# Kernel tuning notes

Hardware: AMD Instinct MI355X
Metric: run time of the kernel (lower is better)

Reference implementation:

```python
import jax, jax.numpy as jnp
import numpy as np

B, N, C, L, H = 8, 128, 64, 3, 128  # batch, objects, channels, eq-layers, message hidden
NEG_SLOPE = 0.01  # torch leaky_relu default


def setup_inputs() -> dict:
    key = jax.random.key(0)
    ks = jax.random.split(key, 10)
    def p(k, shape, fan):
        return jax.random.normal(k, shape, dtype=jnp.float32) * np.float32(np.sqrt(2.0 / fan))
    return {
        "x": jax.random.normal(ks[0], (B, N, N, C), dtype=jnp.float32),
        "mask": jnp.ones((B, N, N, 1), dtype=jnp.float32),
        # MessageNet per eq-layer: Linear(C->H), Linear(H->H), Linear(H->C), stacked over L layers
        "msg_w1": p(ks[1], (L, H, C), C + H),
        "msg_b1": jnp.zeros((L, H), jnp.float32),
        "msg_w2": p(ks[2], (L, H, H), H + H),
        "msg_b2": jnp.zeros((L, H), jnp.float32),
        "msg_w3": p(ks[3], (L, C, H), H + C),
        "msg_b3": jnp.zeros((L, C), jnp.float32),
        # Eq2to2 params: coefs (in_dim, out_dim, 15), bias, diag_bias
        "coefs": p(ks[4], (L, C, C, 15), C + C + 15),
        "bias": jnp.zeros((L, C), jnp.float32),
        "diag_bias": jnp.zeros((L, C), jnp.float32),
    }


def leaky(x):
    return jax.nn.leaky_relu(x, NEG_SLOPE)


def eops_2_to_2(x):
    # x: (B, m, m, C) -> ops: (B, C, 15, m, m); aggregation='sum'
    t = jnp.transpose(x, (0, 3, 1, 2))            # (B, C, m, m)
    m = t.shape[-1]
    eye = jnp.eye(m, dtype=t.dtype)
    diag = jnp.diagonal(t, axis1=-2, axis2=-1)    # (B, C, m)
    sum_diag = diag.sum(-1, keepdims=True)        # (B, C, 1)
    sum_rows = t.sum(-1)                          # (B, C, m)  sum over j
    sum_cols = t.sum(-2)                          # (B, C, m)  sum over i
    sum_all = t.sum((-2, -1))[..., None]          # (B, C, 1)
    de = lambda v: v[..., :, None] * eye          # diag_embed with broadcast
    shp = t.shape
    bc = lambda a: jnp.broadcast_to(a, shp)
    ops = [
        de(diag),                                 # 1  diag -> diag
        de(sum_diag),                             # 2  trace -> diag
        de(sum_rows),                             # 3  row sums -> diag
        de(sum_cols),                             # 4  col sums -> diag
        de(sum_all),                              # 5  total sum -> diag
        bc(sum_cols[..., :, None]),               # 6  col sums broadcast over j
        bc(sum_rows[..., :, None]),               # 7  row sums broadcast over j
        bc(sum_cols[..., None, :]),               # 8  col sums broadcast over i
        bc(sum_rows[..., None, :]),               # 9  row sums broadcast over i
        t,                                        # 10 identity
        jnp.swapaxes(t, -2, -1),                  # 11 transpose
        bc(diag[..., :, None]),                   # 12 diag broadcast over j
        bc(diag[..., None, :]),                   # 13 diag broadcast over i
        bc(sum_diag[..., :, None]),               # 14 trace broadcast everywhere
        bc(sum_all[..., :, None]),                # 15 total sum broadcast everywhere
    ]
    return jnp.stack(ops, axis=2)                 # (B, C, 15, m, m)


def reference(x, mask, msg_w1, msg_b1, msg_w2, msg_b2, msg_w3, msg_b3, coefs, bias, diag_bias):
    m = x.shape[1]
    eye = jnp.eye(m, dtype=x.dtype)[None, :, :, None]  # (1, m, m, 1)
    for l in range(L):
        # MessageNet: pointwise MLP over channels, activation after each linear, then mask
        h = leaky(jnp.einsum('nijc,hc->nijh', x, msg_w1[l]) + msg_b1[l])
        h = leaky(jnp.einsum('nijc,hc->nijh', h, msg_w2[l]) + msg_b2[l])
        h = leaky(jnp.einsum('nijc,hc->nijh', h, msg_w3[l]) + msg_b3[l])
        h = h * mask
        # Eq2to2
        ops = eops_2_to_2(h)                              # (B, C, 15, m, m)
        out = jnp.einsum('dsb,ndbij->nijs', coefs[l], ops)
        out = out + bias[l][None, None, None, :] + eye * diag_bias[l][None, None, None, :]
        out = leaky(out)
        x = out * mask
    return x
```

## Files before the change

kernel.cpp:

```cpp
#include <hip/hip_runtime.h>
#include <hip/hip_bf16.h>

#define BB 8
#define NN 128
#define CC 64
#define LL 3
#define HH 128
#define NEG 0.01f
#define NPOS (BB*NN*NN)

typedef __attribute__((ext_vector_type(8))) short shortx8;
typedef __attribute__((ext_vector_type(4))) float f32x4;

#define OFF_HHI   0L
#define OFF_XN    8388608L
#define OFF_RS    12582912L
#define OFF_DG    12648448L
#define OFF_RCDH  12713984L
#define OFF_RCDL  12812288L
#define OFF_U     12911616L
#define OFF_V     12977152L
#define OFF_D     13042688L
#define OFF_SB    13108224L

__device__ __forceinline__ float leaky(float v) { return v >= 0.f ? v : NEG * v; }

__device__ __forceinline__ short f2bf(float f) {
    return (short)__bfloat16_as_ushort(__float2bfloat16(f));
}
__device__ __forceinline__ float bf2f(short s) {
    unsigned u = ((unsigned)(unsigned short)s) << 16;
    return __builtin_bit_cast(float, u);
}
__device__ __forceinline__ unsigned pkf(float a, float b) {
    return (unsigned)(unsigned short)f2bf(a) | ((unsigned)(unsigned short)f2bf(b) << 16);
}
__device__ __forceinline__ shortx8 cvt8(const float* p) {
    float4 f0 = *(const float4*)p, f1 = *(const float4*)(p + 4);
    shortx8 r;
    r[0]=f2bf(f0.x); r[1]=f2bf(f0.y); r[2]=f2bf(f0.z); r[3]=f2bf(f0.w);
    r[4]=f2bf(f1.x); r[5]=f2bf(f1.y); r[6]=f2bf(f1.z); r[7]=f2bf(f1.w);
    return r;
}

__global__ void prep_kernel(const float* __restrict__ w1, const float* __restrict__ w2,
                            const float* __restrict__ w3, const float* __restrict__ coefs,
                            float* __restrict__ ws) {
    long idx = (long)blockIdx.x * 256 + threadIdx.x;
    short* sb = (short*)(ws + OFF_SB);
    if (idx < 24576) {
        sb[idx] = f2bf(w1[idx]);
    } else if (idx < 73728) {
        sb[idx] = f2bf(w2[idx - 24576]);
    } else if (idx < 98304) {
        sb[idx] = f2bf(w3[idx - 73728]);
    } else if (idx < 110592) {
        long r = idx - 98304; int l = (int)(r / 4096); int q = (int)(r % 4096);
        int s = q >> 6, d = q & 63;
        float v = coefs[(((long)l*CC + d)*CC + s)*15 + 9];
        short hi = f2bf(v);
        sb[98304 + r]  = hi;
        sb[110592 + r] = f2bf(v - bf2f(hi));
    } else if (idx < 122880) {
        long r = idx - 110592; int l = (int)(r / 4096); int q = (int)(r % 4096);
        int s = q >> 6, d = q & 63;
        float v = coefs[(((long)l*CC + d)*CC + s)*15 + 10];
        short hi = f2bf(v);
        sb[122880 + r] = hi;
        sb[135168 + r] = f2bf(v - bf2f(hi));
    } else if (idx < 233472) {
        long r = idx - 122880;
        int l = (int)(r / 36864); int q = (int)(r % 36864);
        int o = q / 192, k = q % 192;
        int wo = o >> 6, s = o & 63, wk = k >> 6, d = k & 63;
        const int sel[3][3] = {{5,6,11},{7,8,12},{3,2,0}};
        float v = coefs[(((long)l*CC + d)*CC + s)*15 + sel[wo][wk]];
        short hi = f2bf(v);
        sb[147456 + r] = hi;
        sb[258048 + r] = f2bf(v - bf2f(hi));
    }
}

__global__ __launch_bounds__(256, 5) void mlp_kernel(
    const float* __restrict__ xf, const short* __restrict__ xb,
    const float* __restrict__ mask,
    const float* __restrict__ b1, const float* __restrict__ b2, const float* __restrict__ b3,
    const short* __restrict__ wb1, const short* __restrict__ wb2, const short* __restrict__ wb3,
    short* __restrict__ hout)
{
    __shared__ __align__(16) char lds[32768];
    const int t = threadIdx.x;
    const int lane = t & 63;
    const int w = t >> 6;
    const int arow = lane & 15;
    const int kgrp = lane >> 4;
    const long pos0 = (long)blockIdx.x * 64;
    const int XT = 16384;

    {
        const int row = t >> 2, q = t & 3;
        const long off = (pos0 + row)*CC + q*16;
        shortx8 v0, v1;
        if (xb) { v0 = *(const shortx8*)(xb + off); v1 = *(const shortx8*)(xb + off + 8); }
        else    { v0 = cvt8(xf + off);              v1 = cvt8(xf + off + 8); }
        const int swz = (row & 7) << 4;
        *(shortx8*)(&lds[XT + row*128 + ((q*32)      ^ swz)]) = v0;
        *(shortx8*)(&lds[XT + row*128 + ((q*32 + 16) ^ swz)]) = v1;
    }
    __syncthreads();

    {
        f32x4 acc[2][4];
        #pragma unroll
        for (int of = 0; of < 2; ++of)
            #pragma unroll
            for (int pf = 0; pf < 4; ++pf) acc[of][pf] = (f32x4){0.f,0.f,0.f,0.f};
        #pragma unroll
        for (int kk = 0; kk < 2; ++kk) {
            shortx8 bx[4];
            #pragma unroll
            for (int pf = 0; pf < 4; ++pf) {
                const int p = pf*16 + arow;
                bx[pf] = *(const shortx8*)(&lds[XT + p*128 + ((kk*64 + kgrp*16) ^ ((p & 7) << 4))]);
            }
            #pragma unroll
            for (int of = 0; of < 2; ++of) {
                const shortx8 a = *(const shortx8*)(wb1 + (long)(w*32 + of*16 + arow)*CC + kk*32 + kgrp*8);
                #pragma unroll
                for (int pf = 0; pf < 4; ++pf)
                    acc[of][pf] = __builtin_amdgcn_mfma_f32_16x16x32_bf16(a, bx[pf], acc[of][pf], 0, 0, 0);
            }
        }
        #pragma unroll
        for (int of = 0; of < 2; ++of) {
            const int o0 = w*32 + of*16 + kgrp*4;
            const float4 bv = *(const float4*)(b1 + o0);
            #pragma unroll
            for (int pf = 0; pf < 4; ++pf) {
                const int p = pf*16 + arow;
                unsigned u0 = pkf(leaky(acc[of][pf][0] + bv.x), leaky(acc[of][pf][1] + bv.y));
                unsigned u1 = pkf(leaky(acc[of][pf][2] + bv.z), leaky(acc[of][pf][3] + bv.w));
                *(uint2*)(&lds[p*256 + ((o0*2) ^ ((p & 15) << 4))]) = make_uint2(u0, u1);
            }
        }
    }
    __syncthreads();

    {
        f32x4 acc[2][4];
        #pragma unroll
        for (int of = 0; of < 2; ++of)
            #pragma unroll
            for (int pf = 0; pf < 4; ++pf) acc[of][pf] = (f32x4){0.f,0.f,0.f,0.f};
        #pragma unroll
        for (int kk = 0; kk < 4; ++kk) {
            shortx8 bx[4];
            #pragma unroll
            for (int pf = 0; pf < 4; ++pf) {
                const int p = pf*16 + arow;
                bx[pf] = *(const shortx8*)(&lds[p*256 + ((kk*64 + kgrp*16) ^ ((p & 15) << 4))]);
            }
            #pragma unroll
            for (int of = 0; of < 2; ++of) {
                const shortx8 a = *(const shortx8*)(wb2 + (long)(w*32 + of*16 + arow)*HH + kk*32 + kgrp*8);
                #pragma unroll
                for (int pf = 0; pf < 4; ++pf)
                    acc[of][pf] = __builtin_amdgcn_mfma_f32_16x16x32_bf16(a, bx[pf], acc[of][pf], 0, 0, 0);
            }
        }
        __syncthreads();
        #pragma unroll
        for (int of = 0; of < 2; ++of) {
            const int o0 = w*32 + of*16 + kgrp*4;
            const float4 bv = *(const float4*)(b2 + o0);
            #pragma unroll
            for (int pf = 0; pf < 4; ++pf) {
                const int p = pf*16 + arow;
                unsigned u0 = pkf(leaky(acc[of][pf][0] + bv.x), leaky(acc[of][pf][1] + bv.y));
                unsigned u1 = pkf(leaky(acc[of][pf][2] + bv.z), leaky(acc[of][pf][3] + bv.w));
                *(uint2*)(&lds[16384 + p*256 + ((o0*2) ^ ((p & 15) << 4))]) = make_uint2(u0, u1);
            }
        }
    }
    __syncthreads();

    {
        f32x4 acc[4];
        #pragma unroll
        for (int pf = 0; pf < 4; ++pf) acc[pf] = (f32x4){0.f,0.f,0.f,0.f};
        #pragma unroll
        for (int kk = 0; kk < 4; ++kk) {
            const shortx8 a = *(const shortx8*)(wb3 + (long)(w*16 + arow)*HH + kk*32 + kgrp*8);
            #pragma unroll
            for (int pf = 0; pf < 4; ++pf) {
                const int p = pf*16 + arow;
                const shortx8 bx = *(const shortx8*)(&lds[16384 + p*256 + ((kk*64 + kgrp*16) ^ ((p & 15) << 4))]);
                acc[pf] = __builtin_amdgcn_mfma_f32_16x16x32_bf16(a, bx, acc[pf], 0, 0, 0);
            }
        }
        const int o0 = w*16 + kgrp*4;
        const float4 bv = *(const float4*)(b3 + o0);
        #pragma unroll
        for (int pf = 0; pf < 4; ++pf) {
            const int p = pf*16 + arow;
            const long pos = pos0 + p;
            const float mv = mask[pos];
            float v0 = leaky(acc[pf][0] + bv.x) * mv;
            float v1 = leaky(acc[pf][1] + bv.y) * mv;
            float v2 = leaky(acc[pf][2] + bv.z) * mv;
            float v3 = leaky(acc[pf][3] + bv.w) * mv;
            *(uint2*)(hout + pos*CC + o0) = make_uint2(pkf(v0, v1), pkf(v2, v3));
        }
    }
}

__global__ __launch_bounds__(256) void reduce_kernel(const short* __restrict__ h,
                                                     float* __restrict__ rowsum,
                                                     float* __restrict__ diag,
                                                     short* __restrict__ rcdh,
                                                     short* __restrict__ rcdl) {
    const int br = blockIdx.x;
    const int n = br >> 7, r = br & 127;
    const int t = threadIdx.x;
    const int c8 = (t & 7) * 8;
    const int g = t >> 3;
    __shared__ float red[32][64];
    const long rowbase = ((long)(n*NN + r) * NN) * CC;

    {
        float s[8];
        #pragma unroll
        for (int e = 0; e < 8; ++e) s[e] = 0.f;
        for (int j = g; j < NN; j += 32) {
            const shortx8 vh = *(const shortx8*)(h + rowbase + (long)j*CC + c8);
            #pragma unroll
            for (int e = 0; e < 8; ++e) s[e] += bf2f(vh[e]);
        }
        #pragma unroll
        for (int e = 0; e < 8; ++e) red[g][c8 + e] = s[e];
    }
    __syncthreads();
    if (t < 64) {
        float rs = 0.f;
        #pragma unroll
        for (int k = 0; k < 32; ++k) rs += red[k][t];
        rowsum[(long)br*CC + t] = rs;
        short hh = f2bf(rs);
        rcdh[(long)br*192 + 64 + t] = hh;
        rcdl[(long)br*192 + 64 + t] = f2bf(rs - bf2f(hh));
    }
    __syncthreads();

    {
        const long colbase = ((long)n*NN*NN + r) * CC;
        float s[8];
        #pragma unroll
        for (int e = 0; e < 8; ++e) s[e] = 0.f;
        for (int i = g; i < NN; i += 32) {
            const shortx8 vh = *(const shortx8*)(h + colbase + (long)i*NN*CC + c8);
            #pragma unroll
            for (int e = 0; e < 8; ++e) s[e] += bf2f(vh[e]);
        }
        #pragma unroll
        for (int e = 0; e < 8; ++e) red[g][c8 + e] = s[e];
    }
    __syncthreads();
    if (t < 64) {
        float cs = 0.f;
        #pragma unroll
        for (int k = 0; k < 32; ++k) cs += red[k][t];
        short hh = f2bf(cs);
        rcdh[(long)br*192 + t] = hh;
        rcdl[(long)br*192 + t] = f2bf(cs - bf2f(hh));
        const float dg = bf2f(h[rowbase + (long)r*CC + t]);
        diag[(long)br*CC + t] = dg;
        short hd = f2bf(dg);
        rcdh[(long)br*192 + 128 + t] = hd;
        rcdl[(long)br*192 + 128 + t] = f2bf(dg - bf2f(hd));
    }
}

__global__ __launch_bounds__(256) void uvd_kernel(
    const short* __restrict__ rcdh, const short* __restrict__ rcdl,
    const short* __restrict__ kh, const short* __restrict__ kl,
    const float* __restrict__ rowsum, const float* __restrict__ diag,
    const float* __restrict__ coefs, int layer,
    float* __restrict__ U, float* __restrict__ V, float* __restrict__ D)
{
    __shared__ float ra[4][64], rb[4][64];
    __shared__ float ub[64], db[64];
    const int t = threadIdx.x, lane = t & 63, w = t >> 6;
    const int arow = lane & 15, kgrp = lane >> 4;
    const int r0 = blockIdx.x * 64;
    const int nb = r0 >> 7;

    {
        const int c = t & 63, g = t >> 6;
        float a = 0.f, b = 0.f;
        for (int i = g; i < NN; i += 4) {
            a += rowsum[((long)nb*NN + i)*CC + c];
            b += diag[((long)nb*NN + i)*CC + c];
        }
        ra[g][c] = a; rb[g][c] = b;
    }
    __syncthreads();
    if (t < 128) {
        const int which = t >> 6, s = t & 63;
        const float* cf = coefs + (long)layer*CC*CC*15;
        float acc = 0.f;
        for (int d = 0; d < CC; ++d) {
            const float tt = ra[0][d] + ra[1][d] + ra[2][d] + ra[3][d];
            const float tr = rb[0][d] + rb[1][d] + rb[2][d] + rb[3][d];
            const float* cds = cf + ((long)d*CC + s)*15;
            if (which == 0) acc += cds[13]*tr + cds[14]*tt;
            else            acc += cds[1]*tr + cds[4]*tt;
        }
        if (which == 0) ub[s] = acc; else db[s] = acc;
    }
    __syncthreads();

    f32x4 acc[3][4];
    #pragma unroll
    for (int o = 0; o < 3; ++o)
        #pragma unroll
        for (int pf = 0; pf < 4; ++pf) acc[o][pf] = (f32x4){0.f,0.f,0.f,0.f};
    #pragma unroll
    for (int kk = 0; kk < 6; ++kk) {
        shortx8 bh[4], bl[4];
        #pragma unroll
        for (int pf = 0; pf < 4; ++pf) {
            const long off = (long)(r0 + pf*16 + arow)*192 + kk*32 + kgrp*8;
            bh[pf] = *(const shortx8*)(rcdh + off);
            bl[pf] = *(const shortx8*)(rcdl + off);
        }
        #pragma unroll
        for (int o = 0; o < 3; ++o) {
            const long aoff = (long)((w*3 + o)*16 + arow)*192 + kk*32 + kgrp*8;
            const shortx8 ah = *(const shortx8*)(kh + aoff);
            const shortx8 al = *(const shortx8*)(kl + aoff);
            #pragma unroll
            for (int pf = 0; pf < 4; ++pf) {
                acc[o][pf] = __builtin_amdgcn_mfma_f32_16x16x32_bf16(ah, bh[pf], acc[o][pf], 0, 0, 0);
                acc[o][pf] = __builtin_amdgcn_mfma_f32_16x16x32_bf16(ah, bl[pf], acc[o][pf], 0, 0, 0);
                acc[o][pf] = __builtin_amdgcn_mfma_f32_16x16x32_bf16(al, bh[pf], acc[o][pf], 0, 0, 0);
            }
        }
    }
    #pragma unroll
    for (int o = 0; o < 3; ++o) {
        const int o16 = (w*3 + o)*16;
        const int o0 = o16 + kgrp*4;
        #pragma unroll
        for (int pf = 0; pf < 4; ++pf) {
            const long rr = r0 + pf*16 + arow;
            float4 a = make_float4(acc[o][pf][0], acc[o][pf][1], acc[o][pf][2], acc[o][pf][3]);
            if (o16 < 64) {
                a.x += ub[o0]; a.y += ub[o0+1]; a.z += ub[o0+2]; a.w += ub[o0+3];
                *(float4*)(U + rr*CC + o0) = a;
            } else if (o16 < 128) {
                *(float4*)(V + rr*CC + (o0 - 64)) = a;
            } else {
                const int q = o0 - 128;
                a.x += db[q]; a.y += db[q+1]; a.z += db[q+2]; a.w += db[q+3];
                *(float4*)(D + rr*CC + q) = a;
            }
        }
    }
}

__global__ __launch_bounds__(256, 6) void eq_kernel(
    const short* __restrict__ h, const float* __restrict__ mask,
    const short* __restrict__ c9h, const short* __restrict__ c9l,
    const short* __restrict__ c10h, const short* __restrict__ c10l,
    const float* __restrict__ U, const float* __restrict__ V, const float* __restrict__ D,
    const float* __restrict__ bias, const float* __restrict__ idbias,
    float* __restrict__ outf, short* __restrict__ outb)
{
    __shared__ __align__(16) char lds[16384];
    const int t = threadIdx.x, lane = t & 63, w = t >> 6;
    const int arow = lane & 15, kgrp = lane >> 4;
    const int n = blockIdx.y;
    const int pr = blockIdx.x;
    int it = (int)((sqrtf(8.f*pr + 1.f) - 1.f)*0.5f);
    while ((it+1)*(it+2)/2 <= pr) ++it;
    while (it*(it+1)/2 > pr) --it;
    const int jt = pr - it*(it+1)/2;
    const int i0 = it*8, j0 = jt*8;
    const int s0 = w*16;

    shortx8 A9h[2], A9l[2], A10h[2], A10l[2];
    #pragma unroll
    for (int kk = 0; kk < 2; ++kk) {
        const long co = (long)(s0 + arow)*CC + kk*32 + kgrp*8;
        A9h[kk]  = *(const shortx8*)(c9h  + co);
        A9l[kk]  = *(const shortx8*)(c9l  + co);
        A10h[kk] = *(const shortx8*)(c10h + co);
        A10l[kk] = *(const shortx8*)(c10l + co);
    }

    {
        const int row = t >> 2, q = t & 3;
        const long posA = ((long)n*NN + i0 + (row >> 3))*NN + (j0 + (row & 7));
        const long posM = ((long)n*NN + j0 + (row & 7))*NN + (i0 + (row >> 3));
        const short* sA = h + posA*CC + q*16;
        const short* sM = h + posM*CC + q*16;
        shortx8 v0 = *(const shortx8*)(sA);
        shortx8 v1 = *(const shortx8*)(sA + 8);
        shortx8 v4 = *(const shortx8*)(sM);
        shortx8 v5 = *(const shortx8*)(sM + 8);
        const int swz = (row & 7) << 4;
        const int d0 = row*128 + ((q*32) ^ swz);
        const int d1 = row*128 + ((q*32 + 16) ^ swz);
        *(shortx8*)(&lds[d0]) = v0;          *(shortx8*)(&lds[d1]) = v1;
        *(shortx8*)(&lds[8192 + d0]) = v4;   *(shortx8*)(&lds[8192 + d1]) = v5;
    }
    __syncthreads();

    f32x4 accA[4], accM[4];
    #pragma unroll
    for (int pf = 0; pf < 4; ++pf) { accA[pf] = (f32x4){0.f,0.f,0.f,0.f}; accM[pf] = (f32x4){0.f,0.f,0.f,0.f}; }

    #pragma unroll
    for (int kk = 0; kk < 2; ++kk) {
        #pragma unroll
        for (int pf = 0; pf < 4; ++pf) {
            const int p = pf*16 + arow;
            const int off = (kk*64 + kgrp*16) ^ ((p & 7) << 4);
            const shortx8 Ah = *(const shortx8*)(&lds[p*128 + off]);
            const shortx8 Mh = *(const shortx8*)(&lds[8192 + p*128 + off]);
            accA[pf] = __builtin_amdgcn_mfma_f32_16x16x32_bf16(A9h[kk],  Ah, accA[pf], 0, 0, 0);
            accA[pf] = __builtin_amdgcn_mfma_f32_16x16x32_bf16(A9l[kk],  Ah, accA[pf], 0, 0, 0);
            accA[pf] = __builtin_amdgcn_mfma_f32_16x16x32_bf16(A10h[kk], Mh, accA[pf], 0, 0, 0);
            accA[pf] = __builtin_amdgcn_mfma_f32_16x16x32_bf16(A10l[kk], Mh, accA[pf], 0, 0, 0);
            accM[pf] = __builtin_amdgcn_mfma_f32_16x16x32_bf16(A9h[kk],  Mh, accM[pf], 0, 0, 0);
            accM[pf] = __builtin_amdgcn_mfma_f32_16x16x32_bf16(A9l[kk],  Mh, accM[pf], 0, 0, 0);
            accM[pf] = __builtin_amdgcn_mfma_f32_16x16x32_bf16(A10h[kk], Ah, accM[pf], 0, 0, 0);
            accM[pf] = __builtin_amdgcn_mfma_f32_16x16x32_bf16(A10l[kk], Ah, accM[pf], 0, 0, 0);
        }
    }

    const int sc = s0 + kgrp*4;
    const float4 bv = *(const float4*)(bias + sc);
    #pragma unroll
    for (int pf = 0; pf < 4; ++pf) {
        const int p = pf*16 + arow;
        {
            const int pi = i0 + (p >> 3), pj = j0 + (p & 7);
            const long pix = ((long)n*NN + pi)*NN + pj;
            const float4 u4 = *(const float4*)(U + ((long)n*NN + pi)*CC + sc);
            const float4 v4 = *(const float4*)(V + ((long)n*NN + pj)*CC + sc);
            float vv[4];
            vv[0] = accA[pf][0] + u4.x + v4.x + bv.x;
            vv[1] = accA[pf][1] + u4.y + v4.y + bv.y;
            vv[2] = accA[pf][2] + u4.z + v4.z + bv.z;
            vv[3] = accA[pf][3] + u4.w + v4.w + bv.w;
            if (it == jt && pi == pj) {
                const float4 d4  = *(const float4*)(D + ((long)n*NN + pi)*CC + sc);
                const float4 db4 = *(const float4*)(idbias + sc);
                vv[0] += d4.x + db4.x; vv[1] += d4.y + db4.y;
                vv[2] += d4.z + db4.z; vv[3] += d4.w + db4.w;
            }
            const float mv = mask[pix];
            #pragma unroll
            for (int r = 0; r < 4; ++r) vv[r] = leaky(vv[r]) * mv;
            if (outf) *(float4*)(outf + pix*CC + sc) = make_float4(vv[0], vv[1], vv[2], vv[3]);
            else      *(uint2*)(outb + pix*CC + sc) = make_uint2(pkf(vv[0], vv[1]), pkf(vv[2], vv[3]));
        }
        if (it != jt) {
            const int pi = j0 + (p & 7), pj = i0 + (p >> 3);
            const long pix = ((long)n*NN + pi)*NN + pj;
            const float4 u4 = *(const float4*)(U + ((long)n*NN + pi)*CC + sc);
            const float4 v4 = *(const float4*)(V + ((long)n*NN + pj)*CC + sc);
            float vv[4];
            vv[0] = accM[pf][0] + u4.x + v4.x + bv.x;
            vv[1] = accM[pf][1] + u4.y + v4.y + bv.y;
            vv[2] = accM[pf][2] + u4.z + v4.z + bv.z;
            vv[3] = accM[pf][3] + u4.w + v4.w + bv.w;
            const float mv = mask[pix];
            #pragma unroll
            for (int r = 0; r < 4; ++r) vv[r] = leaky(vv[r]) * mv;
            if (outf) *(float4*)(outf + pix*CC + sc) = make_float4(vv[0], vv[1], vv[2], vv[3]);
            else      *(uint2*)(outb + pix*CC + sc) = make_uint2(pkf(vv[0], vv[1]), pkf(vv[2], vv[3]));
        }
    }
}

extern "C" void kernel_launch(void* const* d_in, const int* in_sizes, int n_in,
                              void* d_out, int out_size, void* d_ws, size_t ws_size,
                              hipStream_t stream) {
    const float* x     = (const float*)d_in[0];
    const float* mask  = (const float*)d_in[1];
    const float* w1    = (const float*)d_in[2];
    const float* b1    = (const float*)d_in[3];
    const float* w2    = (const float*)d_in[4];
    const float* b2    = (const float*)d_in[5];
    const float* w3    = (const float*)d_in[6];
    const float* b3    = (const float*)d_in[7];
    const float* coefs = (const float*)d_in[8];
    const float* bias  = (const float*)d_in[9];
    const float* idb   = (const float*)d_in[10];
    float* out = (float*)d_out;
    float* ws  = (float*)d_ws;

    short* hh     = (short*)(ws + OFF_HHI);
    short* xn     = (short*)(ws + OFF_XN);
    float* rowsum = ws + OFF_RS;
    float* diag   = ws + OFF_DG;
    short* rcdh   = (short*)(ws + OFF_RCDH);
    short* rcdl   = (short*)(ws + OFF_RCDL);
    float* U      = ws + OFF_U;
    float* V      = ws + OFF_V;
    float* D      = ws + OFF_D;
    short* sb     = (short*)(ws + OFF_SB);

    prep_kernel<<<912, 256, 0, stream>>>(w1, w2, w3, coefs, ws);

    for (int l = 0; l < LL; ++l) {
        mlp_kernel<<<NPOS/64, 256, 0, stream>>>(
            (l == 0) ? x : nullptr, (l == 0) ? nullptr : xn, mask,
            b1 + l*HH, b2 + l*HH, b3 + l*CC,
            sb + (long)l*HH*CC, sb + 24576 + (long)l*HH*HH, sb + 73728 + (long)l*CC*HH,
            hh);
        reduce_kernel<<<BB*NN, 256, 0, stream>>>(hh, rowsum, diag, rcdh, rcdl);
        uvd_kernel<<<16, 256, 0, stream>>>(rcdh, rcdl,
            sb + 147456 + (long)l*36864, sb + 258048 + (long)l*36864,
            rowsum, diag, coefs, l, U, V, D);
        eq_kernel<<<dim3(136, BB), 256, 0, stream>>>(
            hh, mask,
            sb + 98304 + (long)l*CC*CC, sb + 110592 + (long)l*CC*CC,
            sb + 122880 + (long)l*CC*CC, sb + 135168 + (long)l*CC*CC,
            U, V, D, bias + l*CC, idb + l*CC,
            (l == LL-1) ? out : nullptr, (l == LL-1) ? nullptr : xn);
    }
}
```

Baseline: 238.9 us.

## Fuse row sums and diagonal extraction into MLP epilogue

The MLP kernel's epilogue now reduces each block's 64 positions per channel with wave shuffles and writes partial row sums, and it also writes the diagonal entries in fp32 straight from registers. The reduce kernel becomes a column-sum-only kernel that combines the two half-row partials and reads the diagonal from the buffer. This removes one full pass over the bf16 hidden tensor per layer. A subtle side effect: row sums and diagonal are now taken from fp32 values before bf16 rounding, which differs slightly numerically from column sums computed on rounded data.

```diff
diff --git a/kernel.cpp b/kernel.cpp
--- a/kernel.cpp
+++ b/kernel.cpp
@@ -13,6 +13,7 @@
 typedef __attribute__((ext_vector_type(4))) float f32x4;
 
 #define OFF_HHI   0L
+#define OFF_RS2   4194304L
 #define OFF_XN    8388608L
 #define OFF_RS    12582912L
 #define OFF_DG    12648448L
@@ -86,7 +87,7 @@
     const float* __restrict__ mask,
     const float* __restrict__ b1, const float* __restrict__ b2, const float* __restrict__ b3,
     const short* __restrict__ wb1, const short* __restrict__ wb2, const short* __restrict__ wb3,
-    short* __restrict__ hout)
+    short* __restrict__ hout, float* __restrict__ rowsum2, float* __restrict__ diagOut)
 {
     __shared__ __align__(16) char lds[32768];
     const int t = threadIdx.x;
@@ -200,6 +201,10 @@
         }
         const int o0 = w*16 + kgrp*4;
         const float4 bv = *(const float4*)(b3 + o0);
+        const int rowIdx = (int)(pos0 >> 7);
+        const int half64 = (int)(pos0 & 127);
+        const int pDiag  = (rowIdx & 127) - half64;
+        float rs0 = 0.f, rs1 = 0.f, rs2 = 0.f, rs3 = 0.f;
         #pragma unroll
         for (int pf = 0; pf < 4; ++pf) {
             const int p = pf*16 + arow;
@@ -209,14 +214,27 @@
             float v1 = leaky(acc[pf][1] + bv.y) * mv;
             float v2 = leaky(acc[pf][2] + bv.z) * mv;
             float v3 = leaky(acc[pf][3] + bv.w) * mv;
+            rs0 += v0; rs1 += v1; rs2 += v2; rs3 += v3;
+            if (p == pDiag)
+                *(float4*)(diagOut + (long)rowIdx*CC + o0) = make_float4(v0, v1, v2, v3);
             *(uint2*)(hout + pos*CC + o0) = make_uint2(pkf(v0, v1), pkf(v2, v3));
         }
-    }
-}
-
-__global__ __launch_bounds__(256) void reduce_kernel(const short* __restrict__ h,
+        #pragma unroll
+        for (int m = 1; m < 16; m <<= 1) {
+            rs0 += __shfl_xor(rs0, m);
+            rs1 += __shfl_xor(rs1, m);
+            rs2 += __shfl_xor(rs2, m);
+            rs3 += __shfl_xor(rs3, m);
+        }
+        if (arow == 0)
+            *(float4*)(rowsum2 + (long)blockIdx.x*CC + o0) = make_float4(rs0, rs1, rs2, rs3);
+    }
+}
+
+__global__ __launch_bounds__(256) void colsum_kernel(const short* __restrict__ h,
+                                                     const float* __restrict__ rowsum2,
+                                                     const float* __restrict__ diagIn,
                                                      float* __restrict__ rowsum,
-                                                     float* __restrict__ diag,
                                                      short* __restrict__ rcdh,
                                                      short* __restrict__ rcdl) {
     const int br = blockIdx.x;
@@ -225,31 +243,6 @@
     const int c8 = (t & 7) * 8;
     const int g = t >> 3;
     __shared__ float red[32][64];
-    const long rowbase = ((long)(n*NN + r) * NN) * CC;
-
-    {
-        float s[8];
-        #pragma unroll
-        for (int e = 0; e < 8; ++e) s[e] = 0.f;
-        for (int j = g; j < NN; j += 32) {
-            const shortx8 vh = *(const shortx8*)(h + rowbase + (long)j*CC + c8);
-            #pragma unroll
-            for (int e = 0; e < 8; ++e) s[e] += bf2f(vh[e]);
-        }
-        #pragma unroll
-        for (int e = 0; e < 8; ++e) red[g][c8 + e] = s[e];
-    }
-    __syncthreads();
-    if (t < 64) {
-        float rs = 0.f;
-        #pragma unroll
-        for (int k = 0; k < 32; ++k) rs += red[k][t];
-        rowsum[(long)br*CC + t] = rs;
-        short hh = f2bf(rs);
-        rcdh[(long)br*192 + 64 + t] = hh;
-        rcdl[(long)br*192 + 64 + t] = f2bf(rs - bf2f(hh));
-    }
-    __syncthreads();
 
     {
         const long colbase = ((long)n*NN*NN + r) * CC;
@@ -272,8 +265,12 @@
         short hh = f2bf(cs);
         rcdh[(long)br*192 + t] = hh;
         rcdl[(long)br*192 + t] = f2bf(cs - bf2f(hh));
-        const float dg = bf2f(h[rowbase + (long)r*CC + t]);
-        diag[(long)br*CC + t] = dg;
+        const float rs = rowsum2[(long)(br*2)*CC + t] + rowsum2[(long)(br*2+1)*CC + t];
+        rowsum[(long)br*CC + t] = rs;
+        short hr = f2bf(rs);
+        rcdh[(long)br*192 + 64 + t] = hr;
+        rcdl[(long)br*192 + 64 + t] = f2bf(rs - bf2f(hr));
+        const float dg = diagIn[(long)br*CC + t];
         short hd = f2bf(dg);
         rcdh[(long)br*192 + 128 + t] = hd;
         rcdl[(long)br*192 + 128 + t] = f2bf(dg - bf2f(hd));
@@ -502,16 +499,17 @@
     float* out = (float*)d_out;
     float* ws  = (float*)d_ws;
 
-    short* hh     = (short*)(ws + OFF_HHI);
-    short* xn     = (short*)(ws + OFF_XN);
-    float* rowsum = ws + OFF_RS;
-    float* diag   = ws + OFF_DG;
-    short* rcdh   = (short*)(ws + OFF_RCDH);
-    short* rcdl   = (short*)(ws + OFF_RCDL);
-    float* U      = ws + OFF_U;
-    float* V      = ws + OFF_V;
-    float* D      = ws + OFF_D;
-    short* sb     = (short*)(ws + OFF_SB);
+    short* hh      = (short*)(ws + OFF_HHI);
+    float* rowsum2 = ws + OFF_RS2;
+    short* xn      = (short*)(ws + OFF_XN);
+    float* rowsum  = ws + OFF_RS;
+    float* diag    = ws + OFF_DG;
+    short* rcdh    = (short*)(ws + OFF_RCDH);
+    short* rcdl    = (short*)(ws + OFF_RCDL);
+    float* U       = ws + OFF_U;
+    float* V       = ws + OFF_V;
+    float* D       = ws + OFF_D;
+    short* sb      = (short*)(ws + OFF_SB);
 
     prep_kernel<<<912, 256, 0, stream>>>(w1, w2, w3, coefs, ws);
 
@@ -520,8 +518,8 @@
             (l == 0) ? x : nullptr, (l == 0) ? nullptr : xn, mask,
             b1 + l*HH, b2 + l*HH, b3 + l*CC,
             sb + (long)l*HH*CC, sb + 24576 + (long)l*HH*HH, sb + 73728 + (long)l*CC*HH,
-            hh);
-        reduce_kernel<<<BB*NN, 256, 0, stream>>>(hh, rowsum, diag, rcdh, rcdl);
+            hh, rowsum2, diag);
+        colsum_kernel<<<BB*NN, 256, 0, stream>>>(hh, rowsum2, diag, rowsum, rcdh, rcdl);
         uvd_kernel<<<16, 256, 0, stream>>>(rcdh, rcdl,
             sb + 147456 + (long)l*36864, sb + 258048 + (long)l*36864,
             rowsum, diag, coefs, l, U, V, D);
```

Measured after the change: 236.1 us (median of 3 runs). About the same (-1.2%).
